# Performance work log

Hardware: AMD Instinct MI355X
Metric: run time of the kernel (lower is better)

Reference implementation:

```python
import jax, jax.numpy as jnp
import numpy as np

H = 8  # heads
EPS = 1e-5


def adaln(x, t, W, b):
    # AdaLayerNorm: emb = Linear(t); scale, shift = chunk(emb, 2, dim=-1)
    emb = t @ W + b                      # [B,1,2*D]
    scale, shift = jnp.split(emb, 2, axis=-1)
    mu = jnp.mean(x, axis=-1, keepdims=True)
    var = jnp.var(x, axis=-1, keepdims=True)
    xn = (x - mu) / jnp.sqrt(var + EPS)  # elementwise_affine=False
    return xn * (1.0 + scale) + shift


def attention(x, ctx, Wq, Wk, Wv, Wo, bo):
    B, N, D = x.shape
    d = D // H
    q = (x @ Wq).reshape(B, N, H, d).transpose(0, 2, 1, 3)          # [B,H,N,d]
    k = (ctx @ Wk).reshape(B, ctx.shape[1], H, d).transpose(0, 2, 1, 3)
    v = (ctx @ Wv).reshape(B, ctx.shape[1], H, d).transpose(0, 2, 1, 3)
    sim = jnp.einsum('bhid,bhjd->bhij', q, k) * (d ** -0.5)
    attn = jax.nn.softmax(sim, axis=-1)
    out = jnp.einsum('bhij,bhjd->bhid', attn, v)
    out = out.transpose(0, 2, 1, 3).reshape(B, N, D)
    return out @ Wo + bo


def geglu_ff(x, W1, b1, W2, b2):
    u, g = jnp.split(x @ W1 + b1, 2, axis=-1)
    return (u * jax.nn.gelu(g, approximate=False)) @ W2 + b2


def setup_inputs() -> dict:
    key = jax.random.key(0)
    ks = jax.random.split(key, 16)
    D = 512
    s = 0.02
    inp = {
        'x': jax.random.normal(ks[0], (2, 2048, D), jnp.float32),
        't': jax.random.normal(ks[1], (2, 1, D), jnp.float32),
        'cond': jax.random.normal(ks[2], (2, 1024, D), jnp.float32),
        'n1_w': jax.random.normal(ks[3], (D, 2 * D), jnp.float32) * s,
        'n1_b': jnp.zeros((2 * D,), jnp.float32),
        'n2_w': jax.random.normal(ks[4], (D, 2 * D), jnp.float32) * s,
        'n2_b': jnp.zeros((2 * D,), jnp.float32),
        'n4_w': jax.random.normal(ks[5], (D, 2 * D), jnp.float32) * s,
        'n4_b': jnp.zeros((2 * D,), jnp.float32),
        'a1_q': jax.random.normal(ks[6], (D, D), jnp.float32) * s,
        'a1_k': jax.random.normal(ks[7], (D, D), jnp.float32) * s,
        'a1_v': jax.random.normal(ks[8], (D, D), jnp.float32) * s,
        'a1_o': jax.random.normal(ks[9], (D, D), jnp.float32) * s,
        'a1_ob': jnp.zeros((D,), jnp.float32),
        'a2_q': jax.random.normal(ks[10], (D, D), jnp.float32) * s,
        'a2_k': jax.random.normal(ks[11], (D, D), jnp.float32) * s,
        'a2_v': jax.random.normal(ks[12], (D, D), jnp.float32) * s,
        'a2_o': jax.random.normal(ks[13], (D, D), jnp.float32) * s,
        'a2_ob': jnp.zeros((D,), jnp.float32),
        'ff_w1': jax.random.normal(ks[14], (D, 8 * D), jnp.float32) * s,
        'ff_b1': jnp.zeros((8 * D,), jnp.float32),
        'ff_w2': jax.random.normal(ks[15], (4 * D, D), jnp.float32) * s,
        'ff_b2': jnp.zeros((D,), jnp.float32),
    }
    return inp


def reference(x, t, cond, n1_w, n1_b, n2_w, n2_b, n4_w, n4_b,
              a1_q, a1_k, a1_v, a1_o, a1_ob,
              a2_q, a2_k, a2_v, a2_o, a2_ob,
              ff_w1, ff_b1, ff_w2, ff_b2):
    # BasicTransformerBlock, is_deform=False, withT=False, inference (dropout/droppath = identity, LayerScale = identity since init_values=0)
    h = adaln(x, t, n1_w, n1_b)
    x = attention(h, h, a1_q, a1_k, a1_v, a1_o, a1_ob) + x
    h = adaln(x, t, n2_w, n2_b)
    x = attention(h, cond, a2_q, a2_k, a2_v, a2_o, a2_ob) + x
    h = adaln(x, t, n4_w, n4_b)
    x = geglu_ff(h, ff_w1, ff_b1, ff_w2, ff_b2) + x
    return x
```

## Files before the change

### kernel.cpp

```cpp
#include <hip/hip_runtime.h>
#include <math.h>

#define D_MODEL 512
#define NHEADS  8
#define DHEAD   64

typedef __bf16  bf16x2 __attribute__((ext_vector_type(2)));
typedef __bf16  bf16x4 __attribute__((ext_vector_type(4)));
typedef __bf16  bf16x8 __attribute__((ext_vector_type(8)));
typedef float   f32x4  __attribute__((ext_vector_type(4)));

__device__ __forceinline__ void gload16(const __bf16* g, __bf16* l) {
    __builtin_amdgcn_global_load_lds(
        (const __attribute__((address_space(1))) unsigned int*)g,
        (__attribute__((address_space(3))) unsigned int*)l, 16, 0, 0);
}

__device__ __forceinline__ void transpose_tile(
        const float* __restrict__ src, __bf16* __restrict__ dst,
        int K, int N, int k0, int n0) {
    __shared__ float t[64][65];
    int tid = threadIdx.x;
    int r = tid >> 6, c = tid & 63;
#pragma unroll
    for (int i = 0; i < 16; ++i)
        t[r + 4 * i][c] = src[(size_t)(k0 + r + 4 * i) * N + n0 + c];
    __syncthreads();
#pragma unroll
    for (int i = 0; i < 16; ++i)
        dst[(size_t)(n0 + r + 4 * i) * K + k0 + c] = (__bf16)t[c][r + 4 * i];
}

struct PrepArgs {
    const float *t, *n1w, *n1b, *n2w, *n2b, *n4w, *n4b;
    float* emb;
    const float* ws[8]; __bf16* wd[8];
    const float *ffw1, *ffw2;
    __bf16 *ff1t, *ff2t;
    const float* cond; __bf16* cbf;
    int B, condN;
};

__global__ __launch_bounds__(256) void prep_kernel(PrepArgs a) {
    int bb = blockIdx.x, tid = threadIdx.x;
    if (bb < 24) {
        int gI = bb * 256 + tid;
        int per = a.B * 2 * D_MODEL;
        if (gI >= 3 * per) return;
        int norm = gI / per;
        int rem  = gI - norm * per;
        int b = rem / (2 * D_MODEL);
        int c = rem % (2 * D_MODEL);
        const float* W  = (norm == 0) ? a.n1w : (norm == 1 ? a.n2w : a.n4w);
        const float* bb_= (norm == 0) ? a.n1b : (norm == 1 ? a.n2b : a.n4b);
        const float* trow = a.t + (size_t)b * D_MODEL;
        float acc = bb_[c];
        for (int k = 0; k < D_MODEL; ++k)
            acc = fmaf(trow[k], W[(size_t)k * (2 * D_MODEL) + c], acc);
        a.emb[gI] = acc;
    } else if (bb < 536) {
        int w = (bb - 24) >> 6, tI = (bb - 24) & 63;
        transpose_tile(a.ws[w], a.wd[w], 512, 512, (tI >> 3) << 6, (tI & 7) << 6);
    } else if (bb < 1048) {
        int tI = bb - 536;
        transpose_tile(a.ffw1, a.ff1t, 512, 4096, (tI & 7) << 6, (tI >> 3) << 6);
    } else if (bb < 1304) {
        int tI = bb - 1048;
        transpose_tile(a.ffw2, a.ff2t, 2048, 512, (tI >> 3) << 6, (tI & 7) << 6);
    } else {
        int i = ((bb - 1304) * 256 + tid) * 4;
        if (i >= a.condN) return;
        float4 v = *(const float4*)(a.cond + i);
        bf16x2 p0, p1;
        p0[0] = (__bf16)v.x; p0[1] = (__bf16)v.y;
        p1[0] = (__bf16)v.z; p1[1] = (__bf16)v.w;
        *(bf16x2*)(a.cbf + i)     = p0;
        *(bf16x2*)(a.cbf + i + 2) = p1;
    }
}

__global__ __launch_bounds__(256) void adaln_apply_kernel(
        const float* __restrict__ x, const float* __restrict__ emb_n,
        __bf16* __restrict__ h, int N) {
    int row = blockIdx.x;
    int b = row / N;
    const float* xr = x + (size_t)row * D_MODEL;
    int tid = threadIdx.x;
    float2 v = *(const float2*)(xr + 2 * tid);
    float s = v.x + v.y, sq = v.x * v.x + v.y * v.y;
#pragma unroll
    for (int off = 32; off; off >>= 1) {
        s  += __shfl_xor(s, off);
        sq += __shfl_xor(sq, off);
    }
    __shared__ float rs[4], rq[4];
    if ((tid & 63) == 0) { rs[tid >> 6] = s; rq[tid >> 6] = sq; }
    __syncthreads();
    float tot  = rs[0] + rs[1] + rs[2] + rs[3];
    float totq = rq[0] + rq[1] + rq[2] + rq[3];
    float mu  = tot * (1.0f / D_MODEL);
    float var = totq * (1.0f / D_MODEL) - mu * mu;
    float inv = rsqrtf(var + 1e-5f);
    const float* er = emb_n + (size_t)b * (2 * D_MODEL);
    float2 sc = *(const float2*)(er + 2 * tid);
    float2 sh = *(const float2*)(er + D_MODEL + 2 * tid);
    bf16x2 o;
    o[0] = (__bf16)((v.x - mu) * inv * (1.0f + sc.x) + sh.x);
    o[1] = (__bf16)((v.y - mu) * inv * (1.0f + sc.y) + sh.y);
    *(bf16x2*)(h + (size_t)row * D_MODEL + 2 * tid) = o;
}

template<int OUT, int WM>
__global__ __launch_bounds__(256) void gemm_bf16_kernel(
        const __bf16* __restrict__ A, const __bf16* __restrict__ Bt,
        const float* __restrict__ bias, const float* __restrict__ res,
        void* __restrict__ Cv, int M, int K, int N) {
    constexpr int BM = 2 * WM;
    constexpr int MI = WM / 16;
    __shared__ __attribute__((aligned(16))) __bf16 As[BM * 64];
    __shared__ __attribute__((aligned(16))) __bf16 Bs[64 * 64];
    int tid = threadIdx.x;
    int wave = tid >> 6, lane = tid & 63;
    int wr = wave >> 1, wc = wave & 1;
    int r = lane & 15, g = lane >> 4;
    int rx = r & 7;
    int m0 = blockIdx.y * BM, n0 = blockIdx.x << 6;

    int lrow = lane >> 3;
    int lcol = ((lane & 7) ^ lrow) << 3;
    const __bf16* Ag = A  + (size_t)(m0 + (wave << 3) + lrow) * K + lcol;
    const __bf16* Bg = Bt + (size_t)(n0 + (wave << 3) + lrow) * K + lcol;
    __bf16* AsW = As + (size_t)(wave << 3) * 64;
    __bf16* BsW = Bs + (size_t)(wave << 3) * 64;

    f32x4 acc[MI][2];
#pragma unroll
    for (int mi = 0; mi < MI; ++mi)
#pragma unroll
        for (int ni = 0; ni < 2; ++ni) acc[mi][ni] = (f32x4){0.f, 0.f, 0.f, 0.f};

    for (int k0 = 0; k0 < K; k0 += 64) {
        if (k0) __syncthreads();
#pragma unroll
        for (int i = 0; i < MI; ++i)
            gload16(Ag + (size_t)(i * 32) * K + k0, AsW + i * 32 * 64);
#pragma unroll
        for (int j = 0; j < 2; ++j)
            gload16(Bg + (size_t)(j * 32) * K + k0, BsW + j * 32 * 64);
        __syncthreads();
#pragma unroll
        for (int kk = 0; kk < 2; ++kk) {
            int cs = ((((kk << 2) + g) ^ rx) << 3);
            bf16x8 af[MI], bf_[2];
#pragma unroll
            for (int mi = 0; mi < MI; ++mi)
                af[mi] = *(const bf16x8*)&As[(size_t)(wr * WM + (mi << 4) + r) * 64 + cs];
#pragma unroll
            for (int ni = 0; ni < 2; ++ni)
                bf_[ni] = *(const bf16x8*)&Bs[(size_t)((wc << 5) + (ni << 4) + r) * 64 + cs];
#pragma unroll
            for (int mi = 0; mi < MI; ++mi)
#pragma unroll
                for (int ni = 0; ni < 2; ++ni)
                    acc[mi][ni] = __builtin_amdgcn_mfma_f32_16x16x32_bf16(
                        af[mi], bf_[ni], acc[mi][ni], 0, 0, 0);
        }
    }

#pragma unroll
    for (int mi = 0; mi < MI; ++mi) {
#pragma unroll
        for (int ni = 0; ni < 2; ++ni) {
            int col = n0 + (wc << 5) + (ni << 4) + r;
            float scl = (OUT == 2 && col < 512) ? 0.125f : 1.0f;
#pragma unroll
            for (int rg = 0; rg < 4; ++rg) {
                int row = m0 + wr * WM + (mi << 4) + (g << 2) + rg;
                if (OUT == 1) {
                    float v = acc[mi][ni][rg] + bias[col] + res[(size_t)row * N + col];
                    ((float*)Cv)[(size_t)row * N + col] = v;
                } else {
                    ((__bf16*)Cv)[(size_t)row * N + col] = (__bf16)(acc[mi][ni][rg] * scl);
                }
            }
        }
    }
}

__global__ __launch_bounds__(256) void gemm_geglu_bf16_kernel(
        const __bf16* __restrict__ A, const __bf16* __restrict__ W1t,
        const float* __restrict__ b1, __bf16* __restrict__ gg, int M, int K) {
    const int NOUT = 4 * D_MODEL;
    __shared__ __attribute__((aligned(16))) __bf16 AsL[128 * 64];
    __shared__ __attribute__((aligned(16))) __bf16 BuL[64 * 64];
    __shared__ __attribute__((aligned(16))) __bf16 BgL[64 * 64];
    int tid = threadIdx.x;
    int wave = tid >> 6, lane = tid & 63;
    int wr = wave >> 1, wc = wave & 1;
    int r = lane & 15, g = lane >> 4;
    int rx = r & 7;
    int m0 = blockIdx.y << 7, n0 = blockIdx.x << 6;

    int lrow = lane >> 3;
    int lcol = ((lane & 7) ^ lrow) << 3;
    const __bf16* Ag = A   + (size_t)(m0 + (wave << 3) + lrow) * K + lcol;
    const __bf16* Ug = W1t + (size_t)(n0 + (wave << 3) + lrow) * K + lcol;
    const __bf16* Gg = W1t + (size_t)(NOUT + n0 + (wave << 3) + lrow) * K + lcol;
    __bf16* AsW = AsL + (size_t)(wave << 3) * 64;
    __bf16* BuW = BuL + (size_t)(wave << 3) * 64;
    __bf16* BgW = BgL + (size_t)(wave << 3) * 64;

    f32x4 accu[4][2], accg[4][2];
#pragma unroll
    for (int mi = 0; mi < 4; ++mi)
#pragma unroll
        for (int ni = 0; ni < 2; ++ni) {
            accu[mi][ni] = (f32x4){0.f, 0.f, 0.f, 0.f};
            accg[mi][ni] = (f32x4){0.f, 0.f, 0.f, 0.f};
        }

    for (int k0 = 0; k0 < K; k0 += 64) {
        if (k0) __syncthreads();
#pragma unroll
        for (int i = 0; i < 4; ++i)
            gload16(Ag + (size_t)(i * 32) * K + k0, AsW + i * 32 * 64);
#pragma unroll
        for (int j = 0; j < 2; ++j) {
            gload16(Ug + (size_t)(j * 32) * K + k0, BuW + j * 32 * 64);
            gload16(Gg + (size_t)(j * 32) * K + k0, BgW + j * 32 * 64);
        }
        __syncthreads();
#pragma unroll
        for (int kk = 0; kk < 2; ++kk) {
            int cs = ((((kk << 2) + g) ^ rx) << 3);
            bf16x8 af[4], bu[2], bg[2];
#pragma unroll
            for (int mi = 0; mi < 4; ++mi)
                af[mi] = *(const bf16x8*)&AsL[(size_t)((wr << 6) + (mi << 4) + r) * 64 + cs];
#pragma unroll
            for (int ni = 0; ni < 2; ++ni) {
                bu[ni] = *(const bf16x8*)&BuL[(size_t)((wc << 5) + (ni << 4) + r) * 64 + cs];
                bg[ni] = *(const bf16x8*)&BgL[(size_t)((wc << 5) + (ni << 4) + r) * 64 + cs];
            }
#pragma unroll
            for (int mi = 0; mi < 4; ++mi)
#pragma unroll
                for (int ni = 0; ni < 2; ++ni) {
                    accu[mi][ni] = __builtin_amdgcn_mfma_f32_16x16x32_bf16(
                        af[mi], bu[ni], accu[mi][ni], 0, 0, 0);
                    accg[mi][ni] = __builtin_amdgcn_mfma_f32_16x16x32_bf16(
                        af[mi], bg[ni], accg[mi][ni], 0, 0, 0);
                }
        }
    }

#pragma unroll
    for (int mi = 0; mi < 4; ++mi) {
#pragma unroll
        for (int ni = 0; ni < 2; ++ni) {
            int col = n0 + (wc << 5) + (ni << 4) + r;
            float bu_ = b1[col], bg_ = b1[NOUT + col];
#pragma unroll
            for (int rg = 0; rg < 4; ++rg) {
                int row = m0 + (wr << 6) + (mi << 4) + (g << 2) + rg;
                float u  = accu[mi][ni][rg] + bu_;
                float gv = accg[mi][ni][rg] + bg_;
                float ge = 0.5f * gv * (1.0f + erff(gv * 0.70710678118654752f));
                gg[(size_t)row * NOUT + col] = (__bf16)(u * ge);
            }
        }
    }
}

__global__ __launch_bounds__(256) void attn_mfma_kernel(
        const __bf16* __restrict__ q, const __bf16* __restrict__ k,
        const __bf16* __restrict__ v, __bf16* __restrict__ o,
        int Nq, int Nk, int sq, int skv) {
    __shared__ __attribute__((aligned(16))) __bf16 Ks[64][72];
    __shared__ __attribute__((aligned(16))) __bf16 Vt[64 * 72];
    __shared__ __attribute__((aligned(16))) __bf16 Pl[4][16][72];

    int tid = threadIdx.x;
    int w = tid >> 6, lane = tid & 63;
    int r = lane & 15, g = lane >> 4;

    int nqb = Nq >> 6;
    int qb = blockIdx.x % nqb;
    int hh = (blockIdx.x / nqb) % NHEADS;
    int b  = blockIdx.x / (nqb * NHEADS);

    const __bf16* qp = q + ((size_t)(b * Nq + (qb << 6) + (w << 4) + r)) * sq
                         + hh * DHEAD + (g << 3);
    bf16x8 qf0 = *(const bf16x8*)qp;
    bf16x8 qf1 = *(const bf16x8*)(qp + 32);

    int krow = tid >> 2, kcb = (tid & 3) << 4;
    int va = tid & 31,  vbb = tid >> 5;
    size_t kvbase = (size_t)b * Nk * skv + (size_t)hh * DHEAD;
    const __bf16* kp = k + kvbase + (size_t)krow * skv + kcb;
    const __bf16* vp = v + kvbase + (size_t)(2 * va) * skv + (vbb << 3);

    f32x4 oacc[4];
#pragma unroll
    for (int dt = 0; dt < 4; ++dt) oacc[dt] = (f32x4){0.f, 0.f, 0.f, 0.f};
    float m = -1e30f, l = 0.f;

    bf16x8 kr0 = *(const bf16x8*)kp;
    bf16x8 kr1 = *(const bf16x8*)(kp + 8);
    bf16x8 vr0 = *(const bf16x8*)vp;
    bf16x8 vr1 = *(const bf16x8*)(vp + skv);
    {
        *(bf16x8*)&Ks[krow][kcb]     = kr0;
        *(bf16x8*)&Ks[krow][kcb + 8] = kr1;
        int blk = (va >> 2) ^ vbb;
        int cw  = ((va & 3) << 1);
#pragma unroll
        for (int j = 0; j < 8; ++j) {
            bf16x2 pr; pr[0] = vr0[j]; pr[1] = vr1[j];
            *(bf16x2*)&Vt[(size_t)(8 * vbb + j) * 72 + blk * 8 + cw] = pr;
        }
    }
    __syncthreads();

    int ntiles = Nk >> 6;
    for (int t = 0; t < ntiles; ++t) {
        bool pre = (t + 1 < ntiles);
        if (pre) {
            const __bf16* kp2 = kp + (size_t)(t + 1) * 64 * skv;
            const __bf16* vp2 = vp + (size_t)(t + 1) * 64 * skv;
            kr0 = *(const bf16x8*)kp2;
            kr1 = *(const bf16x8*)(kp2 + 8);
            vr0 = *(const bf16x8*)vp2;
            vr1 = *(const bf16x8*)(vp2 + skv);
        }

        f32x4 sacc[4];
#pragma unroll
        for (int nt = 0; nt < 4; ++nt) sacc[nt] = (f32x4){0.f, 0.f, 0.f, 0.f};
        __builtin_amdgcn_s_setprio(1);
#pragma unroll
        for (int nt = 0; nt < 4; ++nt) {
            bf16x8 kf0 = *(const bf16x8*)&Ks[(nt << 4) + r][g << 3];
            bf16x8 kf1 = *(const bf16x8*)&Ks[(nt << 4) + r][32 + (g << 3)];
            sacc[nt] = __builtin_amdgcn_mfma_f32_16x16x32_bf16(kf0, qf0, sacc[nt], 0, 0, 0);
            sacc[nt] = __builtin_amdgcn_mfma_f32_16x16x32_bf16(kf1, qf1, sacc[nt], 0, 0, 0);
        }
        __builtin_amdgcn_s_setprio(0);

        float mx = sacc[0][0];
#pragma unroll
        for (int nt = 0; nt < 4; ++nt)
#pragma unroll
            for (int rg = 0; rg < 4; ++rg) mx = fmaxf(mx, sacc[nt][rg]);
        mx = fmaxf(mx, __shfl_xor(mx, 16));
        mx = fmaxf(mx, __shfl_xor(mx, 32));
        bool defer = __all(mx <= m + 8.0f);
        float mn = defer ? m : fmaxf(m, mx);
        if (!defer) {
            float al = __expf(m - mn);
            m = mn;
            l *= al;
#pragma unroll
            for (int dt = 0; dt < 4; ++dt)
#pragma unroll
                for (int rg = 0; rg < 4; ++rg) oacc[dt][rg] *= al;
        }
        float sum = 0.f;
#pragma unroll
        for (int nt = 0; nt < 4; ++nt) {
            bf16x4 pk;
#pragma unroll
            for (int rg = 0; rg < 4; ++rg) {
                float p = __expf(sacc[nt][rg] - mn);
                sum += p;
                pk[rg] = (__bf16)p;
            }
            *(bf16x4*)&Pl[w][r][((nt ^ (r & 3)) << 4) + (g << 2)] = pk;
        }
        sum += __shfl_xor(sum, 16);
        sum += __shfl_xor(sum, 32);
        l += sum;

        __builtin_amdgcn_s_setprio(1);
#pragma unroll
        for (int kh = 0; kh < 2; ++kh) {
            int bb_ = (kh << 1) + (g >> 1);
            bf16x8 pa = *(const bf16x8*)&Pl[w][r][((bb_ ^ (r & 3)) << 4) + ((g & 1) << 3)];
#pragma unroll
            for (int dt = 0; dt < 4; ++dt) {
                int row = (dt << 4) + r;
                int blk = ((kh << 2) + g) ^ ((row >> 3) & 7);
                bf16x8 vf = *(const bf16x8*)&Vt[(size_t)row * 72 + (blk << 3)];
                oacc[dt] = __builtin_amdgcn_mfma_f32_16x16x32_bf16(vf, pa, oacc[dt], 0, 0, 0);
            }
        }
        __builtin_amdgcn_s_setprio(0);

        __syncthreads();
        if (pre) {
            *(bf16x8*)&Ks[krow][kcb]     = kr0;
            *(bf16x8*)&Ks[krow][kcb + 8] = kr1;
            int blk = (va >> 2) ^ vbb;
            int cw  = ((va & 3) << 1);
#pragma unroll
            for (int j = 0; j < 8; ++j) {
                bf16x2 pr; pr[0] = vr0[j]; pr[1] = vr1[j];
                *(bf16x2*)&Vt[(size_t)(8 * vbb + j) * 72 + blk * 8 + cw] = pr;
            }
        }
        __syncthreads();
    }

    float inv = 1.0f / l;
    __bf16* ob = o + ((size_t)(b * Nq + (qb << 6) + (w << 4) + r)) * D_MODEL + hh * DHEAD;
#pragma unroll
    for (int dt = 0; dt < 4; ++dt) {
        bf16x4 ov;
#pragma unroll
        for (int rg = 0; rg < 4; ++rg) ov[rg] = (__bf16)(oacc[dt][rg] * inv);
        *(bf16x4*)&ob[(dt << 4) + (g << 2)] = ov;
    }
}

extern "C" void kernel_launch(void* const* d_in, const int* in_sizes, int n_in,
                              void* d_out, int out_size, void* d_ws, size_t ws_size,
                              hipStream_t stream) {
    const float* x    = (const float*)d_in[0];
    const float* t    = (const float*)d_in[1];
    const float* cond = (const float*)d_in[2];
    const float* n1_w = (const float*)d_in[3];
    const float* n1_b = (const float*)d_in[4];
    const float* n2_w = (const float*)d_in[5];
    const float* n2_b = (const float*)d_in[6];
    const float* n4_w = (const float*)d_in[7];
    const float* n4_b = (const float*)d_in[8];
    const float* a1_q = (const float*)d_in[9];
    const float* a1_k = (const float*)d_in[10];
    const float* a1_v = (const float*)d_in[11];
    const float* a1_o = (const float*)d_in[12];
    const float* a1_ob= (const float*)d_in[13];
    const float* a2_q = (const float*)d_in[14];
    const float* a2_k = (const float*)d_in[15];
    const float* a2_v = (const float*)d_in[16];
    const float* a2_o = (const float*)d_in[17];
    const float* a2_ob= (const float*)d_in[18];
    const float* ff_w1= (const float*)d_in[19];
    const float* ff_b1= (const float*)d_in[20];
    const float* ff_w2= (const float*)d_in[21];
    const float* ff_b2= (const float*)d_in[22];
    float* out = (float*)d_out;

    const int B  = in_sizes[1] / D_MODEL;
    const int N  = in_sizes[0] / (B * D_MODEL);
    const int Nc = in_sizes[2] / (B * D_MODEL);
    const int R  = B * N;
    const int Rc = B * Nc;

    char* Wb = (char*)d_ws;
    float* emb   = (float*)Wb;
    __bf16* r1   = (__bf16*)(Wb + 32768);
    __bf16* qkv  = r1;
    __bf16* q2   = r1;
    __bf16* kv2  = r1 + (size_t)R * 512;
    __bf16* gg   = r1;
    __bf16* h_bf = (__bf16*)(Wb + 32768 + 16777216);
    __bf16* c_bf = (__bf16*)(Wb + 32768 + 16777216 + 4194304);
    __bf16* wts  = (__bf16*)(Wb + 32768 + 16777216 + 4194304 + 2097152);
    __bf16* a1_qt = wts;
    __bf16* a1_ot = wts + 3 * 262144;
    __bf16* a2_qt = wts + 4 * 262144;
    __bf16* a2_kt = wts + 5 * 262144;
    __bf16* a2_ot = wts + 7 * 262144;
    __bf16* ff1t  = wts + 8 * 262144;
    __bf16* ff2t  = ff1t + 2097152;

    dim3 blk(256);

    PrepArgs pa;
    pa.t = t; pa.n1w = n1_w; pa.n1b = n1_b; pa.n2w = n2_w; pa.n2b = n2_b;
    pa.n4w = n4_w; pa.n4b = n4_b; pa.emb = emb;
    pa.ws[0] = a1_q; pa.ws[1] = a1_k; pa.ws[2] = a1_v; pa.ws[3] = a1_o;
    pa.ws[4] = a2_q; pa.ws[5] = a2_k; pa.ws[6] = a2_v; pa.ws[7] = a2_o;
    pa.wd[0] = a1_qt; pa.wd[1] = wts + 262144; pa.wd[2] = wts + 2 * 262144; pa.wd[3] = a1_ot;
    pa.wd[4] = a2_qt; pa.wd[5] = a2_kt; pa.wd[6] = wts + 6 * 262144; pa.wd[7] = a2_ot;
    pa.ffw1 = ff_w1; pa.ffw2 = ff_w2; pa.ff1t = ff1t; pa.ff2t = ff2t;
    pa.cond = cond; pa.cbf = c_bf; pa.B = B; pa.condN = Rc * D_MODEL;
    prep_kernel<<<dim3(1304 + (Rc * D_MODEL) / 1024), blk, 0, stream>>>(pa);

    adaln_apply_kernel<<<dim3(R), blk, 0, stream>>>(x, emb, h_bf, N);
    gemm_bf16_kernel<2, 64><<<dim3(24, R / 128), blk, 0, stream>>>(
        h_bf, a1_qt, nullptr, nullptr, qkv, R, 512, 1536);
    attn_mfma_kernel<<<dim3(B * NHEADS * (N / 64)), blk, 0, stream>>>(
        qkv, qkv + 512, qkv + 1024, h_bf, N, N, 1536, 1536);
    gemm_bf16_kernel<1, 32><<<dim3(8, R / 64), blk, 0, stream>>>(
        h_bf, a1_ot, a1_ob, x, out, R, 512, 512);

    adaln_apply_kernel<<<dim3(R), blk, 0, stream>>>(
        out, emb + (size_t)B * 2 * D_MODEL, h_bf, N);
    gemm_bf16_kernel<0, 32><<<dim3(16, Rc / 64), blk, 0, stream>>>(
        c_bf, a2_kt, nullptr, nullptr, kv2, Rc, 512, 1024);
    gemm_bf16_kernel<2, 32><<<dim3(8, R / 64), blk, 0, stream>>>(
        h_bf, a2_qt, nullptr, nullptr, q2, R, 512, 512);
    attn_mfma_kernel<<<dim3(B * NHEADS * (N / 64)), blk, 0, stream>>>(
        q2, kv2, kv2 + 512, h_bf, N, Nc, 512, 1024);
    gemm_bf16_kernel<1, 32><<<dim3(8, R / 64), blk, 0, stream>>>(
        h_bf, a2_ot, a2_ob, out, out, R, 512, 512);

    adaln_apply_kernel<<<dim3(R), blk, 0, stream>>>(
        out, emb + (size_t)2 * B * 2 * D_MODEL, h_bf, N);
    gemm_geglu_bf16_kernel<<<dim3(32, R / 128), blk, 0, stream>>>(
        h_bf, ff1t, ff_b1, gg, R, 512);
    gemm_bf16_kernel<1, 32><<<dim3(8, R / 64), blk, 0, stream>>>(
        gg, ff2t, ff_b2, out, out, R, 2048, 512);
}
```

Before: 229.5 us.

## Double-buffer attention K/V tiles, use exp2 softmax, merge cross-attn Q/KV GEMMs

The attention kernel now keeps two LDS buffers for K and V and processes tiles in pairs, so the QK^T of one tile overlaps the PV product and staging of the other. It also switches to an XOR-swizzled layout without padding. The query scale now folds in log2(e), so softmax can use exp2f, and the lazy-rescale threshold is widened to match. The cross-attention Q and KV projections are merged into one dual GEMM launch, which removes a launch and fills the GPU better. The costs are more LDS per block, more register pressure from the prefetched fragments, and a loop that assumes an even number of tiles.

```diff
diff --git a/kernel.cpp b/kernel.cpp
--- a/kernel.cpp
+++ b/kernel.cpp
@@ -9,6 +9,9 @@
 typedef __bf16  bf16x4 __attribute__((ext_vector_type(4)));
 typedef __bf16  bf16x8 __attribute__((ext_vector_type(8)));
 typedef float   f32x4  __attribute__((ext_vector_type(4)));
+
+#define QSCALE 0.18033688f
+#define DEFER_THR 11.5416f
 
 __device__ __forceinline__ void gload16(const __bf16* g, __bf16* l) {
     __builtin_amdgcn_global_load_lds(
@@ -111,20 +114,18 @@
 }
 
 template<int OUT, int WM>
-__global__ __launch_bounds__(256) void gemm_bf16_kernel(
+__device__ __forceinline__ void gemm_body(
         const __bf16* __restrict__ A, const __bf16* __restrict__ Bt,
         const float* __restrict__ bias, const float* __restrict__ res,
-        void* __restrict__ Cv, int M, int K, int N) {
-    constexpr int BM = 2 * WM;
+        void* __restrict__ Cv, int M, int K, int N, int bx, int by,
+        __bf16* As, __bf16* Bs) {
     constexpr int MI = WM / 16;
-    __shared__ __attribute__((aligned(16))) __bf16 As[BM * 64];
-    __shared__ __attribute__((aligned(16))) __bf16 Bs[64 * 64];
     int tid = threadIdx.x;
     int wave = tid >> 6, lane = tid & 63;
     int wr = wave >> 1, wc = wave & 1;
     int r = lane & 15, g = lane >> 4;
     int rx = r & 7;
-    int m0 = blockIdx.y * BM, n0 = blockIdx.x << 6;
+    int m0 = by * (2 * WM), n0 = bx << 6;
 
     int lrow = lane >> 3;
     int lcol = ((lane & 7) ^ lrow) << 3;
@@ -172,7 +173,7 @@
 #pragma unroll
         for (int ni = 0; ni < 2; ++ni) {
             int col = n0 + (wc << 5) + (ni << 4) + r;
-            float scl = (OUT == 2 && col < 512) ? 0.125f : 1.0f;
+            float scl = (OUT == 2 && col < 512) ? QSCALE : 1.0f;
 #pragma unroll
             for (int rg = 0; rg < 4; ++rg) {
                 int row = m0 + wr * WM + (mi << 4) + (g << 2) + rg;
@@ -184,6 +185,32 @@
                 }
             }
         }
+    }
+}
+
+template<int OUT, int WM>
+__global__ __launch_bounds__(256) void gemm_bf16_kernel(
+        const __bf16* __restrict__ A, const __bf16* __restrict__ Bt,
+        const float* __restrict__ bias, const float* __restrict__ res,
+        void* __restrict__ Cv, int M, int K, int N) {
+    __shared__ __attribute__((aligned(16))) __bf16 As[2 * WM * 64];
+    __shared__ __attribute__((aligned(16))) __bf16 Bs[64 * 64];
+    gemm_body<OUT, WM>(A, Bt, bias, res, Cv, M, K, N, blockIdx.x, blockIdx.y, As, Bs);
+}
+
+__global__ __launch_bounds__(256) void gemm_dual_kernel(
+        const __bf16* A0, const __bf16* B0, __bf16* C0, int M0,
+        const __bf16* A1, const __bf16* B1, __bf16* C1, int M1) {
+    __shared__ __attribute__((aligned(16))) __bf16 As[64 * 64];
+    __shared__ __attribute__((aligned(16))) __bf16 Bs[64 * 64];
+    int nb0 = 8 * (M0 >> 6);
+    if ((int)blockIdx.x < nb0) {
+        gemm_body<2, 32>(A0, B0, nullptr, nullptr, C0, M0, 512, 512,
+                         blockIdx.x & 7, blockIdx.x >> 3, As, Bs);
+    } else {
+        int id = blockIdx.x - nb0;
+        gemm_body<0, 32>(A1, B1, nullptr, nullptr, C1, M1, 512, 1024,
+                         id & 15, id >> 4, As, Bs);
     }
 }
 
@@ -276,13 +303,14 @@
         const __bf16* __restrict__ q, const __bf16* __restrict__ k,
         const __bf16* __restrict__ v, __bf16* __restrict__ o,
         int Nq, int Nk, int sq, int skv) {
-    __shared__ __attribute__((aligned(16))) __bf16 Ks[64][72];
-    __shared__ __attribute__((aligned(16))) __bf16 Vt[64 * 72];
-    __shared__ __attribute__((aligned(16))) __bf16 Pl[4][16][72];
+    __shared__ __attribute__((aligned(16))) __bf16 Ks[2][4096];
+    __shared__ __attribute__((aligned(16))) __bf16 Vt[2][4096];
+    __shared__ __attribute__((aligned(16))) __bf16 Pl[4][1024];
 
     int tid = threadIdx.x;
     int w = tid >> 6, lane = tid & 63;
     int r = lane & 15, g = lane >> 4;
+    int rx = r & 7;
 
     int nqb = Nq >> 6;
     int qb = blockIdx.x % nqb;
@@ -294,59 +322,52 @@
     bf16x8 qf0 = *(const bf16x8*)qp;
     bf16x8 qf1 = *(const bf16x8*)(qp + 32);
 
-    int krow = tid >> 2, kcb = (tid & 3) << 4;
-    int va = tid & 31,  vbb = tid >> 5;
+    int krow = tid >> 2, kp_ = tid & 3;
+    int va = tid & 31, vbb = tid >> 5;
     size_t kvbase = (size_t)b * Nk * skv + (size_t)hh * DHEAD;
-    const __bf16* kp = k + kvbase + (size_t)krow * skv + kcb;
+    const __bf16* kp = k + kvbase + (size_t)krow * skv + (kp_ << 4);
     const __bf16* vp = v + kvbase + (size_t)(2 * va) * skv + (vbb << 3);
+    int kwo0 = krow * 64 + ((((kp_ << 1) | 0) ^ (krow & 7)) << 3);
+    int kwo1 = krow * 64 + ((((kp_ << 1) | 1) ^ (krow & 7)) << 3);
+    int vwb  = vbb * 512 + ((va & 3) << 1);
 
     f32x4 oacc[4];
 #pragma unroll
     for (int dt = 0; dt < 4; ++dt) oacc[dt] = (f32x4){0.f, 0.f, 0.f, 0.f};
     float m = -1e30f, l = 0.f;
-
-    bf16x8 kr0 = *(const bf16x8*)kp;
-    bf16x8 kr1 = *(const bf16x8*)(kp + 8);
-    bf16x8 vr0 = *(const bf16x8*)vp;
-    bf16x8 vr1 = *(const bf16x8*)(vp + skv);
-    {
-        *(bf16x8*)&Ks[krow][kcb]     = kr0;
-        *(bf16x8*)&Ks[krow][kcb + 8] = kr1;
-        int blk = (va >> 2) ^ vbb;
-        int cw  = ((va & 3) << 1);
+    f32x4 saccA[4], saccB[4];
+    bf16x8 kr0, kr1, vr0, vr1;
+    bf16x8 vf[2][4], pa[2];
+
+    auto LOADREG = [&](int t) {
+        const __bf16* kp2 = kp + (size_t)t * 64 * skv;
+        const __bf16* vp2 = vp + (size_t)t * 64 * skv;
+        kr0 = *(const bf16x8*)kp2; kr1 = *(const bf16x8*)(kp2 + 8);
+        vr0 = *(const bf16x8*)vp2; vr1 = *(const bf16x8*)(vp2 + skv);
+    };
+    auto STAGEW = [&](int buf) {
+        *(bf16x8*)&Ks[buf][kwo0] = kr0;
+        *(bf16x8*)&Ks[buf][kwo1] = kr1;
 #pragma unroll
         for (int j = 0; j < 8; ++j) {
             bf16x2 pr; pr[0] = vr0[j]; pr[1] = vr1[j];
-            *(bf16x2*)&Vt[(size_t)(8 * vbb + j) * 72 + blk * 8 + cw] = pr;
-        }
-    }
-    __syncthreads();
-
-    int ntiles = Nk >> 6;
-    for (int t = 0; t < ntiles; ++t) {
-        bool pre = (t + 1 < ntiles);
-        if (pre) {
-            const __bf16* kp2 = kp + (size_t)(t + 1) * 64 * skv;
-            const __bf16* vp2 = vp + (size_t)(t + 1) * 64 * skv;
-            kr0 = *(const bf16x8*)kp2;
-            kr1 = *(const bf16x8*)(kp2 + 8);
-            vr0 = *(const bf16x8*)vp2;
-            vr1 = *(const bf16x8*)(vp2 + skv);
-        }
-
-        f32x4 sacc[4];
+            *(bf16x2*)&Vt[buf][vwb + j * 64 + (((va >> 2) ^ j) << 3)] = pr;
+        }
+    };
+    auto QKT = [&](f32x4 (&sacc)[4], int buf) {
 #pragma unroll
         for (int nt = 0; nt < 4; ++nt) sacc[nt] = (f32x4){0.f, 0.f, 0.f, 0.f};
         __builtin_amdgcn_s_setprio(1);
 #pragma unroll
         for (int nt = 0; nt < 4; ++nt) {
-            bf16x8 kf0 = *(const bf16x8*)&Ks[(nt << 4) + r][g << 3];
-            bf16x8 kf1 = *(const bf16x8*)&Ks[(nt << 4) + r][32 + (g << 3)];
+            bf16x8 kf0 = *(const bf16x8*)&Ks[buf][((nt << 4) + r) * 64 + ((g ^ rx) << 3)];
+            bf16x8 kf1 = *(const bf16x8*)&Ks[buf][((nt << 4) + r) * 64 + (((g + 4) ^ rx) << 3)];
             sacc[nt] = __builtin_amdgcn_mfma_f32_16x16x32_bf16(kf0, qf0, sacc[nt], 0, 0, 0);
             sacc[nt] = __builtin_amdgcn_mfma_f32_16x16x32_bf16(kf1, qf1, sacc[nt], 0, 0, 0);
         }
         __builtin_amdgcn_s_setprio(0);
-
+    };
+    auto SMAX = [&](f32x4 (&sacc)[4]) {
         float mx = sacc[0][0];
 #pragma unroll
         for (int nt = 0; nt < 4; ++nt)
@@ -354,12 +375,10 @@
             for (int rg = 0; rg < 4; ++rg) mx = fmaxf(mx, sacc[nt][rg]);
         mx = fmaxf(mx, __shfl_xor(mx, 16));
         mx = fmaxf(mx, __shfl_xor(mx, 32));
-        bool defer = __all(mx <= m + 8.0f);
-        float mn = defer ? m : fmaxf(m, mx);
-        if (!defer) {
-            float al = __expf(m - mn);
-            m = mn;
-            l *= al;
+        if (!__all(mx <= m + DEFER_THR)) {
+            float mn = fmaxf(m, mx);
+            float al = exp2f(m - mn);
+            m = mn; l *= al;
 #pragma unroll
             for (int dt = 0; dt < 4; ++dt)
 #pragma unroll
@@ -371,44 +390,61 @@
             bf16x4 pk;
 #pragma unroll
             for (int rg = 0; rg < 4; ++rg) {
-                float p = __expf(sacc[nt][rg] - mn);
+                float p = exp2f(sacc[nt][rg] - m);
                 sum += p;
                 pk[rg] = (__bf16)p;
             }
-            *(bf16x4*)&Pl[w][r][((nt ^ (r & 3)) << 4) + (g << 2)] = pk;
+            *(bf16x4*)&Pl[w][r * 64 + ((((nt << 1) | (g >> 1)) ^ rx) << 3) + ((g & 1) << 2)] = pk;
         }
         sum += __shfl_xor(sum, 16);
         sum += __shfl_xor(sum, 32);
         l += sum;
-
+    };
+    auto VFLOAD = [&](int buf) {
+#pragma unroll
+        for (int kh = 0; kh < 2; ++kh) {
+            pa[kh] = *(const bf16x8*)&Pl[w][r * 64 + ((((kh << 2) + g) ^ rx) << 3)];
+#pragma unroll
+            for (int dt = 0; dt < 4; ++dt)
+                vf[kh][dt] = *(const bf16x8*)&Vt[buf][((dt << 4) + r) * 64
+                                                      + ((((kh << 2) + g) ^ rx) << 3)];
+        }
+    };
+    auto PVOP = [&]() {
         __builtin_amdgcn_s_setprio(1);
 #pragma unroll
-        for (int kh = 0; kh < 2; ++kh) {
-            int bb_ = (kh << 1) + (g >> 1);
-            bf16x8 pa = *(const bf16x8*)&Pl[w][r][((bb_ ^ (r & 3)) << 4) + ((g & 1) << 3)];
-#pragma unroll
-            for (int dt = 0; dt < 4; ++dt) {
-                int row = (dt << 4) + r;
-                int blk = ((kh << 2) + g) ^ ((row >> 3) & 7);
-                bf16x8 vf = *(const bf16x8*)&Vt[(size_t)row * 72 + (blk << 3)];
-                oacc[dt] = __builtin_amdgcn_mfma_f32_16x16x32_bf16(vf, pa, oacc[dt], 0, 0, 0);
-            }
-        }
+        for (int kh = 0; kh < 2; ++kh)
+#pragma unroll
+            for (int dt = 0; dt < 4; ++dt)
+                oacc[dt] = __builtin_amdgcn_mfma_f32_16x16x32_bf16(
+                    vf[kh][dt], pa[kh], oacc[dt], 0, 0, 0);
         __builtin_amdgcn_s_setprio(0);
-
+    };
+
+    int ntiles = Nk >> 6;
+    LOADREG(0);
+    STAGEW(0);
+    LOADREG(1);
+    __syncthreads();
+    QKT(saccA, 0);
+
+    for (int t = 0; t + 1 < ntiles; t += 2) {
+        STAGEW(1);
+        if (t + 2 < ntiles) LOADREG(t + 2);
+        SMAX(saccA);
+        VFLOAD(0);
         __syncthreads();
-        if (pre) {
-            *(bf16x8*)&Ks[krow][kcb]     = kr0;
-            *(bf16x8*)&Ks[krow][kcb + 8] = kr1;
-            int blk = (va >> 2) ^ vbb;
-            int cw  = ((va & 3) << 1);
-#pragma unroll
-            for (int j = 0; j < 8; ++j) {
-                bf16x2 pr; pr[0] = vr0[j]; pr[1] = vr1[j];
-                *(bf16x2*)&Vt[(size_t)(8 * vbb + j) * 72 + blk * 8 + cw] = pr;
-            }
-        }
+        QKT(saccB, 1);
+        PVOP();
+        if (t + 2 < ntiles) {
+            STAGEW(0);
+            if (t + 3 < ntiles) LOADREG(t + 3);
+        }
+        SMAX(saccB);
+        VFLOAD(1);
         __syncthreads();
+        if (t + 2 < ntiles) QKT(saccA, 0);
+        PVOP();
     }
 
     float inv = 1.0f / l;
@@ -497,10 +533,8 @@
 
     adaln_apply_kernel<<<dim3(R), blk, 0, stream>>>(
         out, emb + (size_t)B * 2 * D_MODEL, h_bf, N);
-    gemm_bf16_kernel<0, 32><<<dim3(16, Rc / 64), blk, 0, stream>>>(
-        c_bf, a2_kt, nullptr, nullptr, kv2, Rc, 512, 1024);
-    gemm_bf16_kernel<2, 32><<<dim3(8, R / 64), blk, 0, stream>>>(
-        h_bf, a2_qt, nullptr, nullptr, q2, R, 512, 512);
+    gemm_dual_kernel<<<dim3(8 * (R / 64) + 16 * (Rc / 64)), blk, 0, stream>>>(
+        h_bf, a2_qt, q2, R, c_bf, a2_kt, kv2, Rc);
     attn_mfma_kernel<<<dim3(B * NHEADS * (N / 64)), blk, 0, stream>>>(
         q2, kv2, kv2 + 512, h_bf, N, Nc, 512, 1024);
     gemm_bf16_kernel<1, 32><<<dim3(8, R / 64), blk, 0, stream>>>(
```

New measurement: 218.4 us. 1.05x faster.
